# Kernel tuning notes

Measured on AMD Instinct MI355X. Metric: run time of the kernel, lower is better.

Reference implementation:

```python
import jax, jax.numpy as jnp
import numpy as np

N, E, F, K = 20000, 320000, 256, 3


def setup_inputs() -> dict:
    key = jax.random.key(0)
    ks = jax.random.split(key, 10)
    x = jax.random.normal(ks[0], (N, F), jnp.float32)
    edge_index = jax.random.randint(ks[1], (2, E), 0, N)
    edge_weight = jax.random.uniform(ks[2], (E,), jnp.float32)
    h = jax.random.normal(ks[3], (N, F), jnp.float32)
    c = jax.random.normal(ks[4], (N, F), jnp.float32)
    s = 1.0 / np.sqrt(F)
    W = jax.random.normal(ks[5], (4, F, F), jnp.float32) * s        # x->gate (i,f,c,o)
    theta = jax.random.normal(ks[6], (4, K, F, F), jnp.float32) * s  # Cheb weights per gate
    b_conv = jnp.zeros((4, F), jnp.float32)                          # ChebConv biases
    b = jnp.zeros((4, F), jnp.float32)                               # gate biases
    w_c = jax.random.normal(ks[7], (3, F), jnp.float32) * s          # peephole (i,f,o)
    W_cls = jax.random.normal(ks[8], (F, 1), jnp.float32) * s
    b_cls = jnp.zeros((1,), jnp.float32)
    return dict(x=x, edge_index=edge_index, edge_weight=edge_weight, h=h, c=c,
                W=W, theta=theta, b_conv=b_conv, b=b, w_c=w_c, W_cls=W_cls, b_cls=b_cls)


def _cheb(h, src, dst, wnorm, theta_g, b_g):
    # ChebConv with sym normalization, lambda_max=2: L_hat = -D^{-1/2} A D^{-1/2}
    n = h.shape[0]

    def prop(v):  # (L_hat v)[dst] = sum_e wnorm[e] * v[src[e]]
        return jax.ops.segment_sum(wnorm[:, None] * v[src], dst, num_segments=n)

    Tx0 = h
    out = Tx0 @ theta_g[0]
    Tx1 = prop(h)
    out = out + Tx1 @ theta_g[1]
    for k in range(2, theta_g.shape[0]):
        Tx2 = 2.0 * prop(Tx1) - Tx0
        out = out + Tx2 @ theta_g[k]
        Tx0, Tx1 = Tx1, Tx2
    return out + b_g


def _gclstm(x, src, dst, wnorm, h, c, W, theta, b_conv, b, w_c):
    conv = lambda g: _cheb(h, src, dst, wnorm, theta[g], b_conv[g])
    i = jax.nn.sigmoid(x @ W[0] + conv(0) + w_c[0] * c + b[0])
    f = jax.nn.sigmoid(x @ W[1] + conv(1) + w_c[1] * c + b[1])
    t = jnp.tanh(x @ W[2] + conv(2) + b[2])
    c_new = f * c + i * t
    o = jax.nn.sigmoid(x @ W[3] + conv(3) + w_c[2] * c_new + b[3])
    h_new = o * jnp.tanh(c_new)
    return h_new, c_new


def reference(x, edge_index, edge_weight, h, c, W, theta, b_conv, b, w_c, W_cls, b_cls):
    src, dst = edge_index[0], edge_index[1]
    deg = jax.ops.segment_sum(edge_weight, src, num_segments=x.shape[0])
    dis = jnp.where(deg > 0, jax.lax.rsqrt(jnp.maximum(deg, 1e-12)), 0.0)
    wnorm = -dis[src] * edge_weight * dis[dst]
    h0, c0 = _gclstm(x, src, dst, wnorm, h, c, W, theta, b_conv, b, w_c)
    out = jax.nn.relu(h0) @ W_cls + b_cls  # [N, 1]
    return out, h0, c0
```

## Files before the change

### kernel.cpp

```cpp
#include <hip/hip_runtime.h>
#include <stdint.h>

#define FDIM 256
#define KDIM 1024

typedef __attribute__((ext_vector_type(8))) short short8;
typedef __attribute__((ext_vector_type(4))) float floatx4;

#define GLOBAL_AS __attribute__((address_space(1)))
#define LDS_AS    __attribute__((address_space(3)))

static __device__ __forceinline__ unsigned short f2bf(float f) {
    unsigned int u = __float_as_uint(f);
    unsigned int r = (u + 0x7FFFu + ((u >> 16) & 1u)) >> 16;
    return (unsigned short)r;
}
static __device__ __forceinline__ float bf2f(unsigned short s) {
    return __uint_as_float(((unsigned int)s) << 16);
}
static __device__ __forceinline__ float sig(float x) {
    return 1.f / (1.f + __expf(-x));
}


__global__ void k_degcnt(const int* __restrict__ src, const int* __restrict__ dst,
                         const float* __restrict__ ew, float* deg, int* cnt, int e) {
    int i = blockIdx.x * blockDim.x + threadIdx.x;
    if (i < e) {
        atomicAdd(&deg[src[i]], ew[i]);
        atomicAdd(&cnt[dst[i]], 1);
    }
}

__launch_bounds__(1024)
__global__ void k_scan1(const int* __restrict__ cnt, int* __restrict__ offs,
                        int* __restrict__ part, int n) {
    __shared__ int wsum[16];
    int b = blockIdx.x;
    int i = b * 1024 + (int)threadIdx.x;
    int lane = threadIdx.x & 63;
    int wid = threadIdx.x >> 6;
    int x = (i < n) ? cnt[i] : 0;
#pragma unroll
    for (int s = 1; s < 64; s <<= 1) {
        int t = __shfl_up(x, s);
        if (lane >= s) x += t;
    }
    if (lane == 63) wsum[wid] = x;
    __syncthreads();
    if (wid == 0) {
        int y = (lane < 16) ? wsum[lane] : 0;
#pragma unroll
        for (int s = 1; s < 16; s <<= 1) {
            int t = __shfl_up(y, s);
            if (lane >= s) y += t;
        }
        if (lane < 16) wsum[lane] = y;
    }
    __syncthreads();
    int wbase = (wid > 0) ? wsum[wid - 1] : 0;
    if (i < n) offs[i + 1] = wbase + x;
    if (threadIdx.x == 1023) part[b] = wsum[15];
}

__launch_bounds__(1024)
__global__ void k_scan2(int* __restrict__ offs, const int* __restrict__ part, int n) {
    __shared__ int sprefix;
    int b = blockIdx.x;
    if (threadIdx.x < 64) {
        int p = ((int)threadIdx.x < b) ? part[threadIdx.x] : 0;
#pragma unroll
        for (int s = 32; s; s >>= 1) p += __shfl_down(p, s);
        if (threadIdx.x == 0) sprefix = p;
    }
    __syncthreads();
    int i = b * 1024 + (int)threadIdx.x;
    if (i < n) offs[i + 1] += sprefix;
    if (b == 0 && threadIdx.x == 0) offs[0] = 0;
}

__global__ void k_scatter(const int* __restrict__ src, const int* __restrict__ dst,
                          const float* __restrict__ ew, const float* __restrict__ deg,
                          const int* __restrict__ offs, int* cur,
                          int2* __restrict__ csr, int e) {
    int i = blockIdx.x * blockDim.x + threadIdx.x;
    if (i < e) {
        int s = src[i], d = dst[i];
        float ds_ = deg[s], dd = deg[d];
        float rs = ds_ > 0.f ? rsqrtf(fmaxf(ds_, 1e-12f)) : 0.f;
        float rd = dd > 0.f ? rsqrtf(fmaxf(dd, 1e-12f)) : 0.f;
        float wn = -rs * ew[i] * rd;
        int pos = offs[d] + atomicAdd(&cur[d], 1);
        csr[pos] = make_int2(s, __float_as_int(wn));
    }
}


__global__ void k_packA(const float* __restrict__ x, const float* __restrict__ h,
                        unsigned short* __restrict__ A, int n) {
    int t = blockIdx.x * blockDim.x + threadIdx.x;
    int node = t >> 6, q = t & 63;
    if (node >= n) return;
    floatx4 xv = *(const floatx4*)(x + (size_t)node * FDIM + q * 4);
    floatx4 hv = *(const floatx4*)(h + (size_t)node * FDIM + q * 4);
    ushort4 ox, oh;
    ox.x = f2bf(xv[0]); ox.y = f2bf(xv[1]); ox.z = f2bf(xv[2]); ox.w = f2bf(xv[3]);
    oh.x = f2bf(hv[0]); oh.y = f2bf(hv[1]); oh.z = f2bf(hv[2]); oh.w = f2bf(hv[3]);
    *(ushort4*)(A + (size_t)node * KDIM + q * 4) = ox;
    *(ushort4*)(A + (size_t)node * KDIM + FDIM + q * 4) = oh;
}

__global__ void k_packBt(const float* __restrict__ W, const float* __restrict__ theta,
                         unsigned short* __restrict__ Bt) {
    int t = blockIdx.x * blockDim.x + threadIdx.x;
    int p = t >> 10, r = t & 1023;
    int group = p >> 6, gate = (p >> 4) & 3;
    int feat = (group << 4) | (p & 15);
    int kb = r >> 8, rr = r & 255;
    float v;
    if (kb == 0) v = W[((size_t)(gate * FDIM + rr)) * FDIM + feat];
    else         v = theta[((size_t)((gate * 3 + (kb - 1)) * FDIM + rr)) * FDIM + feat];
    Bt[t] = f2bf(v);
}


__launch_bounds__(256)
__global__ void k_prop1(unsigned short* __restrict__ A, const int* __restrict__ offs,
                        const int2* __restrict__ csr, int n) {
    int wid = (blockIdx.x * blockDim.x + threadIdx.x) >> 6;
    int lane = threadIdx.x & 63;
    if (wid >= n) return;
    int half = lane >> 5, l = lane & 31;
    int beg = offs[wid], end = offs[wid + 1];
    float a[8] = {0.f, 0.f, 0.f, 0.f, 0.f, 0.f, 0.f, 0.f};
    int j = beg + half;
    for (; j + 6 < end; j += 8) {
        int2 e0 = csr[j], e1 = csr[j + 2], e2 = csr[j + 4], e3 = csr[j + 6];
        short8 v0 = *(const short8*)(A + (size_t)e0.x * KDIM + FDIM + l * 8);
        short8 v1 = *(const short8*)(A + (size_t)e1.x * KDIM + FDIM + l * 8);
        short8 v2 = *(const short8*)(A + (size_t)e2.x * KDIM + FDIM + l * 8);
        short8 v3 = *(const short8*)(A + (size_t)e3.x * KDIM + FDIM + l * 8);
        float w0 = __int_as_float(e0.y), w1 = __int_as_float(e1.y);
        float w2 = __int_as_float(e2.y), w3 = __int_as_float(e3.y);
#pragma unroll
        for (int k = 0; k < 8; ++k)
            a[k] += w0 * bf2f((unsigned short)v0[k]) + w1 * bf2f((unsigned short)v1[k])
                  + w2 * bf2f((unsigned short)v2[k]) + w3 * bf2f((unsigned short)v3[k]);
    }
    for (; j < end; j += 2) {
        int2 e0 = csr[j];
        float w0 = __int_as_float(e0.y);
        short8 v0 = *(const short8*)(A + (size_t)e0.x * KDIM + FDIM + l * 8);
#pragma unroll
        for (int k = 0; k < 8; ++k) a[k] += w0 * bf2f((unsigned short)v0[k]);
    }
#pragma unroll
    for (int k = 0; k < 8; ++k) a[k] += __shfl_xor(a[k], 32);
    if (half == 0) {
        short8 o;
#pragma unroll
        for (int k = 0; k < 8; ++k) o[k] = (short)f2bf(a[k]);
        *(short8*)(A + (size_t)wid * KDIM + 2 * FDIM + l * 8) = o;
    }
}

__launch_bounds__(256)
__global__ void k_prop2(unsigned short* __restrict__ A, const float* __restrict__ h,
                        const int* __restrict__ offs, const int2* __restrict__ csr, int n) {
    int wid = (blockIdx.x * blockDim.x + threadIdx.x) >> 6;
    int lane = threadIdx.x & 63;
    if (wid >= n) return;
    int half = lane >> 5, l = lane & 31;
    int beg = offs[wid], end = offs[wid + 1];
    float a[8] = {0.f, 0.f, 0.f, 0.f, 0.f, 0.f, 0.f, 0.f};
    int j = beg + half;
    for (; j + 6 < end; j += 8) {
        int2 e0 = csr[j], e1 = csr[j + 2], e2 = csr[j + 4], e3 = csr[j + 6];
        short8 v0 = *(const short8*)(A + (size_t)e0.x * KDIM + 2 * FDIM + l * 8);
        short8 v1 = *(const short8*)(A + (size_t)e1.x * KDIM + 2 * FDIM + l * 8);
        short8 v2 = *(const short8*)(A + (size_t)e2.x * KDIM + 2 * FDIM + l * 8);
        short8 v3 = *(const short8*)(A + (size_t)e3.x * KDIM + 2 * FDIM + l * 8);
        float w0 = __int_as_float(e0.y), w1 = __int_as_float(e1.y);
        float w2 = __int_as_float(e2.y), w3 = __int_as_float(e3.y);
#pragma unroll
        for (int k = 0; k < 8; ++k)
            a[k] += w0 * bf2f((unsigned short)v0[k]) + w1 * bf2f((unsigned short)v1[k])
                  + w2 * bf2f((unsigned short)v2[k]) + w3 * bf2f((unsigned short)v3[k]);
    }
    for (; j < end; j += 2) {
        int2 e0 = csr[j];
        float w0 = __int_as_float(e0.y);
        short8 v0 = *(const short8*)(A + (size_t)e0.x * KDIM + 2 * FDIM + l * 8);
#pragma unroll
        for (int k = 0; k < 8; ++k) a[k] += w0 * bf2f((unsigned short)v0[k]);
    }
#pragma unroll
    for (int k = 0; k < 8; ++k) a[k] += __shfl_xor(a[k], 32);
    if (half == 0) {
        floatx4 hv0 = *(const floatx4*)(h + (size_t)wid * FDIM + l * 8);
        floatx4 hv1 = *(const floatx4*)(h + (size_t)wid * FDIM + l * 8 + 4);
        short8 o;
#pragma unroll
        for (int k = 0; k < 4; ++k) o[k] = (short)f2bf(2.f * a[k] - hv0[k]);
#pragma unroll
        for (int k = 0; k < 4; ++k) o[4 + k] = (short)f2bf(2.f * a[4 + k] - hv1[k]);
        *(short8*)(A + (size_t)wid * KDIM + 3 * FDIM + l * 8) = o;
    }
}


__launch_bounds__(256, 2)
__global__ void k_gemm(const unsigned short* __restrict__ A, const unsigned short* __restrict__ Bt,
                       const float* __restrict__ c, const float* __restrict__ b_conv,
                       const float* __restrict__ b, const float* __restrict__ w_c,
                       const float* __restrict__ Wcls,
                       float* __restrict__ out_h, float* __restrict__ out_c,
                       float* __restrict__ cls_part, int M, int mtiles) {
    __shared__ unsigned short sA[2][128 * 64];
    __shared__ unsigned short sB[2][128 * 64];
    int tid = threadIdx.x;
    int lane = tid & 63;
    int w = tid >> 6;
    int nb = mtiles * 8;
    int bid = blockIdx.x;
    int wg = (bid & 7) * (nb >> 3) + (bid >> 3);
    int mt = wg >> 3;
    int nt = wg & 7;
    int brow = mt * 128, bcol = nt * 128;
    int wr = (w >> 1) * 64, wc = (w & 1) * 64;
    int l15 = lane & 15, l4 = lane >> 4;

    auto STAGE = [&](int kt, int bufi) {
        int k0 = kt * 64;
#pragma unroll
        for (int p = 0; p < 4; ++p) {
            int cch = tid + p * 256;
            int row = cch >> 3, cslot = cch & 7;
            int csrc = cslot ^ (row & 7);
            int grow = brow + row; if (grow >= M) grow = M - 1;
            const unsigned short* g = A + (size_t)grow * KDIM + k0 + csrc * 8;
            __builtin_amdgcn_global_load_lds((const GLOBAL_AS void*)g,
                                             (LDS_AS void*)(sA[bufi] + cch * 8), 16, 0, 0);
        }
#pragma unroll
        for (int p = 0; p < 4; ++p) {
            int cch = tid + p * 256;
            int row = cch >> 3, cslot = cch & 7;
            int csrc = cslot ^ (row & 7);
            const unsigned short* g = Bt + (size_t)(bcol + row) * KDIM + k0 + csrc * 8;
            __builtin_amdgcn_global_load_lds((const GLOBAL_AS void*)g,
                                             (LDS_AS void*)(sB[bufi] + cch * 8), 16, 0, 0);
        }
    };

    floatx4 acc[4][4];
#pragma unroll
    for (int m = 0; m < 4; ++m)
#pragma unroll
        for (int g = 0; g < 4; ++g)
            acc[m][g] = (floatx4){0.f, 0.f, 0.f, 0.f};

    STAGE(0, 0);

    for (int kt = 0; kt < 16; ++kt) {
        int cur = kt & 1;
        if (kt < 15) {
            STAGE(kt + 1, cur ^ 1);
            asm volatile("s_waitcnt vmcnt(8)" ::: "memory");
        } else {
            asm volatile("s_waitcnt vmcnt(0)" ::: "memory");
        }
        __builtin_amdgcn_s_barrier();
        __builtin_amdgcn_sched_barrier(0);

#pragma unroll
        for (int ks = 0; ks < 2; ++ks) {
            short8 af[4], bfr[4];
#pragma unroll
            for (int m = 0; m < 4; ++m) {
                int ra = wr + m * 16 + l15;
                af[m] = *(const short8*)(sA[cur] + ra * 64 + ((ks * 4 + l4) ^ (ra & 7)) * 8);
            }
#pragma unroll
            for (int g = 0; g < 4; ++g) {
                int rb = wc + g * 16 + l15;
                bfr[g] = *(const short8*)(sB[cur] + rb * 64 + ((ks * 4 + l4) ^ (rb & 7)) * 8);
            }
#pragma unroll
            for (int m = 0; m < 4; ++m)
#pragma unroll
                for (int g = 0; g < 4; ++g)
                    acc[m][g] = __builtin_amdgcn_mfma_f32_16x16x32_bf16(af[m], bfr[g], acc[m][g], 0, 0, 0);
        }
        asm volatile("s_waitcnt lgkmcnt(0)" ::: "memory");
        __builtin_amdgcn_sched_barrier(0);
        __builtin_amdgcn_s_barrier();
    }

    int group = (bcol + wc) >> 6;
    int feat = (group << 4) | l15;
    float bc0 = b_conv[feat], bc1 = b_conv[FDIM + feat];
    float bc2 = b_conv[2 * FDIM + feat], bc3 = b_conv[3 * FDIM + feat];
    float bb0 = b[feat], bb1 = b[FDIM + feat];
    float bb2 = b[2 * FDIM + feat], bb3 = b[3 * FDIM + feat];
    float wci = w_c[feat], wcf = w_c[FDIM + feat], wco = w_c[2 * FDIM + feat];
    float wcl = Wcls[feat];

#pragma unroll
    for (int m = 0; m < 4; ++m) {
#pragma unroll
        for (int j = 0; j < 4; ++j) {
            int node = brow + wr + m * 16 + l4 * 4 + j;
            bool ok = node < M;
            int nidx = ok ? node : (M - 1);
            float cv = c[(size_t)nidx * FDIM + feat];
            float iv = sig(acc[m][0][j] + bc0 + wci * cv + bb0);
            float fv = sig(acc[m][1][j] + bc1 + wcf * cv + bb1);
            float tv = tanhf(acc[m][2][j] + bc2 + bb2);
            float cn = fv * cv + iv * tv;
            float ov = sig(acc[m][3][j] + bc3 + wco * cn + bb3);
            float hn = ov * tanhf(cn);
            if (ok) {
                out_h[(size_t)node * FDIM + feat] = hn;
                out_c[(size_t)node * FDIM + feat] = cn;
            }
            float pcls = fmaxf(hn, 0.f) * wcl;
#pragma unroll
            for (int s = 1; s < 16; s <<= 1) pcls += __shfl_xor(pcls, s);
            if (ok && l15 == 0) cls_part[(size_t)node * 16 + group] = pcls;
        }
    }
}

__global__ void k_cls(const float* __restrict__ cls_part, const float* __restrict__ bcls,
                      float* __restrict__ out_cls, int n) {
    int i = blockIdx.x * blockDim.x + threadIdx.x;
    if (i >= n) return;
    const floatx4* p = (const floatx4*)(cls_part + (size_t)i * 16);
    floatx4 v0 = p[0], v1 = p[1], v2 = p[2], v3 = p[3];
    float s = v0[0] + v0[1] + v0[2] + v0[3] + v1[0] + v1[1] + v1[2] + v1[3]
            + v2[0] + v2[1] + v2[2] + v2[3] + v3[0] + v3[1] + v3[2] + v3[3];
    out_cls[i] = s + bcls[0];
}


extern "C" void kernel_launch(void* const* d_in, const int* in_sizes, int n_in,
                              void* d_out, int out_size, void* d_ws, size_t ws_size,
                              hipStream_t stream) {
    const float* x      = (const float*)d_in[0];
    const int*   eidx   = (const int*)d_in[1];
    const float* ew     = (const float*)d_in[2];
    const float* h      = (const float*)d_in[3];
    const float* c      = (const float*)d_in[4];
    const float* W      = (const float*)d_in[5];
    const float* theta  = (const float*)d_in[6];
    const float* b_conv = (const float*)d_in[7];
    const float* b      = (const float*)d_in[8];
    const float* w_c    = (const float*)d_in[9];
    const float* Wcls   = (const float*)d_in[10];
    const float* bcls   = (const float*)d_in[11];

    const int N = in_sizes[0] / FDIM;
    const int E = in_sizes[2];
    const int* src = eidx;
    const int* dst = eidx + E;

    char* ws = (char*)d_ws;
    size_t off = 0;
    auto alloc = [&](size_t bytes) -> void* {
        void* p = ws + off;
        off += (bytes + 255) & ~(size_t)255;
        return p;
    };
    unsigned short* A   = (unsigned short*)alloc((size_t)N * KDIM * 2);
    unsigned short* Bt  = (unsigned short*)alloc((size_t)KDIM * KDIM * 2);
    float* cls_part     = (float*)alloc((size_t)N * 16 * 4);
    float* deg          = (float*)alloc((size_t)N * 4);
    int*   cnt          = (int*)alloc((size_t)N * 4);
    int*   cur          = (int*)alloc((size_t)N * 4);
    int*   offs         = (int*)alloc((size_t)(N + 1) * 4);
    int*   part         = (int*)alloc(64 * 4);
    int2*  csr          = (int2*)alloc((size_t)E * 8);
    (void)ws_size; (void)n_in; (void)out_size;

    float* out_cls = (float*)d_out;
    float* out_h   = out_cls + N;
    float* out_c   = out_h + (size_t)N * FDIM;

    size_t zbytes = (size_t)((char*)(cur + N) - (char*)deg);
    hipMemsetAsync(deg, 0, zbytes, stream);

    int nsb = (N + 1023) / 1024;
    k_degcnt<<<(E + 255) / 256, 256, 0, stream>>>(src, dst, ew, deg, cnt, E);
    k_scan1<<<nsb, 1024, 0, stream>>>(cnt, offs, part, N);
    k_scan2<<<nsb, 1024, 0, stream>>>(offs, part, N);
    k_scatter<<<(E + 255) / 256, 256, 0, stream>>>(src, dst, ew, deg, offs, cur, csr, E);
    k_packA<<<(N * 64 + 255) / 256, 256, 0, stream>>>(x, h, A, N);
    k_packBt<<<(KDIM * KDIM + 255) / 256, 256, 0, stream>>>(W, theta, Bt);
    k_prop1<<<(N * 64 + 255) / 256, 256, 0, stream>>>(A, offs, csr, N);
    k_prop2<<<(N * 64 + 255) / 256, 256, 0, stream>>>(A, h, offs, csr, N);
    int mtiles = (N + 127) / 128;
    k_gemm<<<mtiles * 8, 256, 0, stream>>>(A, Bt, c, b_conv, b, w_c, Wcls,
                                           out_h, out_c, cls_part, N, mtiles);
    k_cls<<<(N + 255) / 256, 256, 0, stream>>>(cls_part, bcls, out_cls, N);
}
```

Measured before the change: 211.7 us.

## Fuse degree counting with packing, single-buffer GEMM, atomically accumulate classifier

Merges the degree/count atomics kernel into the x/h bf16 packing kernel. The classifier partial-sum kernel is removed in favour of atomicAdd into a zeroed output. The GEMM drops LDS double buffering for a single buffer with plain __syncthreads, which permits 3 blocks per CU instead of 2. Launch count goes down, but global-to-LDS loads no longer overlap with MFMA compute, and float atomics make the classifier sum order nondeterministic.

```diff
diff --git a/kernel.cpp b/kernel.cpp
--- a/kernel.cpp
+++ b/kernel.cpp
@@ -23,13 +23,24 @@
 }
 
 
-__global__ void k_degcnt(const int* __restrict__ src, const int* __restrict__ dst,
-                         const float* __restrict__ ew, float* deg, int* cnt, int e) {
-    int i = blockIdx.x * blockDim.x + threadIdx.x;
-    if (i < e) {
-        atomicAdd(&deg[src[i]], ew[i]);
-        atomicAdd(&cnt[dst[i]], 1);
-    }
+__global__ void k_pre(const float* __restrict__ x, const float* __restrict__ h,
+                      unsigned short* __restrict__ A, int n,
+                      const int* __restrict__ src, const int* __restrict__ dst,
+                      const float* __restrict__ ew, float* deg, int* cnt, int e) {
+    int t = blockIdx.x * blockDim.x + threadIdx.x;
+    if (t < e) {
+        atomicAdd(&deg[src[t]], ew[t]);
+        atomicAdd(&cnt[dst[t]], 1);
+    }
+    int node = t >> 6, q = t & 63;
+    if (node >= n) return;
+    floatx4 xv = *(const floatx4*)(x + (size_t)node * FDIM + q * 4);
+    floatx4 hv = *(const floatx4*)(h + (size_t)node * FDIM + q * 4);
+    ushort4 ox, oh;
+    ox.x = f2bf(xv[0]); ox.y = f2bf(xv[1]); ox.z = f2bf(xv[2]); ox.w = f2bf(xv[3]);
+    oh.x = f2bf(hv[0]); oh.y = f2bf(hv[1]); oh.z = f2bf(hv[2]); oh.w = f2bf(hv[3]);
+    *(ushort4*)(A + (size_t)node * KDIM + q * 4) = ox;
+    *(ushort4*)(A + (size_t)node * KDIM + FDIM + q * 4) = oh;
 }
 
 __launch_bounds__(1024)
@@ -93,21 +104,6 @@
         int pos = offs[d] + atomicAdd(&cur[d], 1);
         csr[pos] = make_int2(s, __float_as_int(wn));
     }
-}
-
-
-__global__ void k_packA(const float* __restrict__ x, const float* __restrict__ h,
-                        unsigned short* __restrict__ A, int n) {
-    int t = blockIdx.x * blockDim.x + threadIdx.x;
-    int node = t >> 6, q = t & 63;
-    if (node >= n) return;
-    floatx4 xv = *(const floatx4*)(x + (size_t)node * FDIM + q * 4);
-    floatx4 hv = *(const floatx4*)(h + (size_t)node * FDIM + q * 4);
-    ushort4 ox, oh;
-    ox.x = f2bf(xv[0]); ox.y = f2bf(xv[1]); ox.z = f2bf(xv[2]); ox.w = f2bf(xv[3]);
-    oh.x = f2bf(hv[0]); oh.y = f2bf(hv[1]); oh.z = f2bf(hv[2]); oh.w = f2bf(hv[3]);
-    *(ushort4*)(A + (size_t)node * KDIM + q * 4) = ox;
-    *(ushort4*)(A + (size_t)node * KDIM + FDIM + q * 4) = oh;
 }
 
 __global__ void k_packBt(const float* __restrict__ W, const float* __restrict__ theta,
@@ -209,15 +205,15 @@
 }
 
 
-__launch_bounds__(256, 2)
+__launch_bounds__(256, 3)
 __global__ void k_gemm(const unsigned short* __restrict__ A, const unsigned short* __restrict__ Bt,
                        const float* __restrict__ c, const float* __restrict__ b_conv,
                        const float* __restrict__ b, const float* __restrict__ w_c,
-                       const float* __restrict__ Wcls,
+                       const float* __restrict__ Wcls, const float* __restrict__ bcls,
                        float* __restrict__ out_h, float* __restrict__ out_c,
-                       float* __restrict__ cls_part, int M, int mtiles) {
-    __shared__ unsigned short sA[2][128 * 64];
-    __shared__ unsigned short sB[2][128 * 64];
+                       float* __restrict__ out_cls, int M, int mtiles) {
+    __shared__ unsigned short sA[128 * 64];
+    __shared__ unsigned short sB[128 * 64];
     int tid = threadIdx.x;
     int lane = tid & 63;
     int w = tid >> 6;
@@ -230,7 +226,14 @@
     int wr = (w >> 1) * 64, wc = (w & 1) * 64;
     int l15 = lane & 15, l4 = lane >> 4;
 
-    auto STAGE = [&](int kt, int bufi) {
+    floatx4 acc[4][4];
+#pragma unroll
+    for (int m = 0; m < 4; ++m)
+#pragma unroll
+        for (int g = 0; g < 4; ++g)
+            acc[m][g] = (floatx4){0.f, 0.f, 0.f, 0.f};
+
+    for (int kt = 0; kt < 16; ++kt) {
         int k0 = kt * 64;
 #pragma unroll
         for (int p = 0; p < 4; ++p) {
@@ -240,7 +243,7 @@
             int grow = brow + row; if (grow >= M) grow = M - 1;
             const unsigned short* g = A + (size_t)grow * KDIM + k0 + csrc * 8;
             __builtin_amdgcn_global_load_lds((const GLOBAL_AS void*)g,
-                                             (LDS_AS void*)(sA[bufi] + cch * 8), 16, 0, 0);
+                                             (LDS_AS void*)(sA + cch * 8), 16, 0, 0);
         }
 #pragma unroll
         for (int p = 0; p < 4; ++p) {
@@ -249,29 +252,9 @@
             int csrc = cslot ^ (row & 7);
             const unsigned short* g = Bt + (size_t)(bcol + row) * KDIM + k0 + csrc * 8;
             __builtin_amdgcn_global_load_lds((const GLOBAL_AS void*)g,
-                                             (LDS_AS void*)(sB[bufi] + cch * 8), 16, 0, 0);
-        }
-    };
-
-    floatx4 acc[4][4];
-#pragma unroll
-    for (int m = 0; m < 4; ++m)
-#pragma unroll
-        for (int g = 0; g < 4; ++g)
-            acc[m][g] = (floatx4){0.f, 0.f, 0.f, 0.f};
-
-    STAGE(0, 0);
-
-    for (int kt = 0; kt < 16; ++kt) {
-        int cur = kt & 1;
-        if (kt < 15) {
-            STAGE(kt + 1, cur ^ 1);
-            asm volatile("s_waitcnt vmcnt(8)" ::: "memory");
-        } else {
-            asm volatile("s_waitcnt vmcnt(0)" ::: "memory");
-        }
-        __builtin_amdgcn_s_barrier();
-        __builtin_amdgcn_sched_barrier(0);
+                                             (LDS_AS void*)(sB + cch * 8), 16, 0, 0);
+        }
+        __syncthreads();
 
 #pragma unroll
         for (int ks = 0; ks < 2; ++ks) {
@@ -279,12 +262,12 @@
 #pragma unroll
             for (int m = 0; m < 4; ++m) {
                 int ra = wr + m * 16 + l15;
-                af[m] = *(const short8*)(sA[cur] + ra * 64 + ((ks * 4 + l4) ^ (ra & 7)) * 8);
+                af[m] = *(const short8*)(sA + ra * 64 + ((ks * 4 + l4) ^ (ra & 7)) * 8);
             }
 #pragma unroll
             for (int g = 0; g < 4; ++g) {
                 int rb = wc + g * 16 + l15;
-                bfr[g] = *(const short8*)(sB[cur] + rb * 64 + ((ks * 4 + l4) ^ (rb & 7)) * 8);
+                bfr[g] = *(const short8*)(sB + rb * 64 + ((ks * 4 + l4) ^ (rb & 7)) * 8);
             }
 #pragma unroll
             for (int m = 0; m < 4; ++m)
@@ -292,9 +275,7 @@
                 for (int g = 0; g < 4; ++g)
                     acc[m][g] = __builtin_amdgcn_mfma_f32_16x16x32_bf16(af[m], bfr[g], acc[m][g], 0, 0, 0);
         }
-        asm volatile("s_waitcnt lgkmcnt(0)" ::: "memory");
-        __builtin_amdgcn_sched_barrier(0);
-        __builtin_amdgcn_s_barrier();
+        __syncthreads();
     }
 
     int group = (bcol + wc) >> 6;
@@ -305,6 +286,7 @@
     float bb2 = b[2 * FDIM + feat], bb3 = b[3 * FDIM + feat];
     float wci = w_c[feat], wcf = w_c[FDIM + feat], wco = w_c[2 * FDIM + feat];
     float wcl = Wcls[feat];
+    float bias = (group == 0) ? bcls[0] : 0.f;
 
 #pragma unroll
     for (int m = 0; m < 4; ++m) {
@@ -327,20 +309,9 @@
             float pcls = fmaxf(hn, 0.f) * wcl;
 #pragma unroll
             for (int s = 1; s < 16; s <<= 1) pcls += __shfl_xor(pcls, s);
-            if (ok && l15 == 0) cls_part[(size_t)node * 16 + group] = pcls;
-        }
-    }
-}
-
-__global__ void k_cls(const float* __restrict__ cls_part, const float* __restrict__ bcls,
-                      float* __restrict__ out_cls, int n) {
-    int i = blockIdx.x * blockDim.x + threadIdx.x;
-    if (i >= n) return;
-    const floatx4* p = (const floatx4*)(cls_part + (size_t)i * 16);
-    floatx4 v0 = p[0], v1 = p[1], v2 = p[2], v3 = p[3];
-    float s = v0[0] + v0[1] + v0[2] + v0[3] + v1[0] + v1[1] + v1[2] + v1[3]
-            + v2[0] + v2[1] + v2[2] + v2[3] + v3[0] + v3[1] + v3[2] + v3[3];
-    out_cls[i] = s + bcls[0];
+            if (ok && l15 == 0) atomicAdd(&out_cls[node], pcls + bias);
+        }
+    }
 }
 
 
@@ -374,7 +345,6 @@
     };
     unsigned short* A   = (unsigned short*)alloc((size_t)N * KDIM * 2);
     unsigned short* Bt  = (unsigned short*)alloc((size_t)KDIM * KDIM * 2);
-    float* cls_part     = (float*)alloc((size_t)N * 16 * 4);
     float* deg          = (float*)alloc((size_t)N * 4);
     int*   cnt          = (int*)alloc((size_t)N * 4);
     int*   cur          = (int*)alloc((size_t)N * 4);
@@ -389,18 +359,17 @@
 
     size_t zbytes = (size_t)((char*)(cur + N) - (char*)deg);
     hipMemsetAsync(deg, 0, zbytes, stream);
+    hipMemsetAsync(out_cls, 0, (size_t)N * 4, stream);
 
     int nsb = (N + 1023) / 1024;
-    k_degcnt<<<(E + 255) / 256, 256, 0, stream>>>(src, dst, ew, deg, cnt, E);
+    k_pre<<<(N * 64 + 255) / 256, 256, 0, stream>>>(x, h, A, N, src, dst, ew, deg, cnt, E);
     k_scan1<<<nsb, 1024, 0, stream>>>(cnt, offs, part, N);
     k_scan2<<<nsb, 1024, 0, stream>>>(offs, part, N);
     k_scatter<<<(E + 255) / 256, 256, 0, stream>>>(src, dst, ew, deg, offs, cur, csr, E);
-    k_packA<<<(N * 64 + 255) / 256, 256, 0, stream>>>(x, h, A, N);
-    k_packBt<<<(KDIM * KDIM + 255) / 256, 256, 0, stream>>>(W, theta, Bt);
     k_prop1<<<(N * 64 + 255) / 256, 256, 0, stream>>>(A, offs, csr, N);
     k_prop2<<<(N * 64 + 255) / 256, 256, 0, stream>>>(A, h, offs, csr, N);
+    k_packBt<<<(KDIM * KDIM + 255) / 256, 256, 0, stream>>>(W, theta, Bt);
     int mtiles = (N + 127) / 128;
-    k_gemm<<<mtiles * 8, 256, 0, stream>>>(A, Bt, c, b_conv, b, w_c, Wcls,
-                                           out_h, out_c, cls_part, N, mtiles);
-    k_cls<<<(N + 255) / 256, 256, 0, stream>>>(cls_part, bcls, out_cls, N);
-}
+    k_gemm<<<mtiles * 8, 256, 0, stream>>>(A, Bt, c, b_conv, b, w_c, Wcls, bcls,
+                                           out_h, out_c, out_cls, N, mtiles);
+}
```

Measured after the change: 190.2 us. 10.2% less time.
